# Optimization experiments

Measured on AMD Instinct MI355X. Metric: run time of the kernel, lower is better.

The kernel has to match this reference:

```python
import jax, jax.numpy as jnp
import numpy as np
import math

B, N, D, H, HC = 2, 2048, 1024, 16, 8
HIDDEN = 4 * D
MAX_PERIOD = 10000.0


def _timestep_embedding(t, dim):
    half = dim // 2
    freqs = jnp.exp(-math.log(MAX_PERIOD) * jnp.arange(half, dtype=jnp.float32) / half)
    args = t[:, None] * freqs[None, :]
    return jnp.concatenate([jnp.cos(args), jnp.sin(args)], axis=-1)


def _layer_norm(x, scale, bias, eps=1e-6):
    mu = jnp.mean(x, axis=-1, keepdims=True)
    var = jnp.mean(jnp.square(x - mu), axis=-1, keepdims=True)
    return (x - mu) * jax.lax.rsqrt(var + eps) * scale + bias


def _modulate(x, shift, scale):
    return x * (1.0 + scale[:, None, :]) + shift[:, None, :]


def setup_inputs():
    key = jax.random.key(0)
    ks = jax.random.split(key, 16)

    def dense(k, fin, fout):
        return jax.random.normal(k, (fin, fout), dtype=jnp.float32) / np.sqrt(fin)

    return {
        'x': jax.random.normal(ks[0], (B, N, D), dtype=jnp.float32),
        't': jax.random.uniform(ks[1], (B,), dtype=jnp.float32) * 1000.0,
        'norm1_scale': jnp.ones((D,), jnp.float32),
        'norm1_bias': jnp.zeros((D,), jnp.float32),
        'norm2_scale': jnp.ones((D,), jnp.float32),
        'norm2_bias': jnp.zeros((D,), jnp.float32),
        'tc_w1': dense(ks[2], HIDDEN, HIDDEN),
        'tc_b1': jnp.zeros((HIDDEN,), jnp.float32),
        'tc_w2': dense(ks[3], HIDDEN, HIDDEN),
        'tc_b2': jnp.zeros((HIDDEN,), jnp.float32),
        'tc_wa': 0.02 * dense(ks[4], HIDDEN, 4 * D),
        'tc_ba': jnp.zeros((4 * D,), jnp.float32),
        'tc_wc': 0.02 * dense(ks[5], HIDDEN, 4 * D),
        'tc_bc': jnp.zeros((4 * D,), jnp.float32),
        'attn_qk_w': dense(ks[6], D, D),
        'attn_v_w': dense(ks[7], D, D),
        'attn_out_w': dense(ks[8], D, D),
        'doob_w': 0.02 * dense(ks[9], D, 1),
        'doob_b': jnp.zeros((1,), jnp.float32),
        'ch_qk_w': dense(ks[10], D, D),
        'ch_v_w': dense(ks[11], D, D),
        'ch_out_w': dense(ks[12], D, D),
        'tau': jnp.ones((HC, 1, 1), jnp.float32),
        'gamma1': 1e-4 * jnp.ones((D,), jnp.float32),
        'gamma2': 1e-4 * jnp.ones((D,), jnp.float32),
    }


def reference(x, t, norm1_scale, norm1_bias, norm2_scale, norm2_bias,
              tc_w1, tc_b1, tc_w2, tc_b2, tc_wa, tc_ba, tc_wc, tc_bc,
              attn_qk_w, attn_v_w, attn_out_w, doob_w, doob_b,
              ch_qk_w, ch_v_w, ch_out_w, tau, gamma1, gamma2):
    # ---- AdaLN time conditioning ----
    emb = _timestep_embedding(t, HIDDEN)                 # (B, HIDDEN)
    h = jax.nn.silu(emb @ tc_w1 + tc_b1)
    h = jax.nn.silu(h @ tc_w2 + tc_b2)
    a_shift, a_scale, a_gate, a_lg = jnp.split(h @ tc_wa + tc_ba, 4, axis=-1)
    c_shift, c_scale, c_gate, c_lg = jnp.split(h @ tc_wc + tc_bc, 4, axis=-1)

    # ---- token-diffusion attention (MHDM, tied Q=K, Doob tilt) ----
    x1 = _modulate(_layer_norm(x, norm1_scale, norm1_bias), a_shift, a_scale)
    qk = (x1 @ attn_qk_w) * jnp.exp(a_lg)[:, None, :]    # (B,N,D)
    v = x1 @ attn_v_w
    dh = D // H
    qh = qk.reshape(B, N, H, dh).transpose(0, 2, 1, 3)   # (B,H,N,dh)
    vh = v.reshape(B, N, H, dh).transpose(0, 2, 1, 3)
    dot = jnp.einsum('bhmd,bhnd->bhmn', qh, qh)
    q2 = jnp.sum(qh * qh, axis=-1)
    logits = 2.0 * dot - q2[:, :, :, None] - q2[:, :, None, :]
    phi = (x1 @ doob_w + doob_b)[..., 0]                 # (B,N) destination tilt
    logits = logits + phi[:, None, None, :]
    attn = jax.nn.softmax(logits, axis=-1)
    w = jnp.einsum('bhmn,bhnd->bhmd', attn, vh)
    attn_out = w.transpose(0, 2, 1, 3).reshape(B, N, D) @ attn_out_w
    x = x + attn_out * a_gate[:, None, :] * gamma1

    # ---- channel-diffusion attention ----
    x2 = _modulate(_layer_norm(x, norm2_scale, norm2_bias), c_shift, c_scale)
    qkc = (x2 @ ch_qk_w) * jnp.exp(c_lg)[:, None, :]
    vc = x2 @ ch_v_w
    dhc = D // HC
    qkc = qkc.transpose(0, 2, 1).reshape(B, HC, dhc, N)  # (B,HC,dhc,N)
    vc = vc.transpose(0, 2, 1).reshape(B, HC, dhc, N)
    dotc = jnp.einsum('bhcn,bhdn->bhcd', qkc, qkc)
    q2c = jnp.sum(qkc * qkc, axis=-1)                    # (B,HC,dhc)
    logitsc = (2.0 * dotc - q2c[:, :, :, None] - q2c[:, :, None, :]) / math.sqrt(N)
    logitsc = logitsc * tau[None, ...]
    attnc = jax.nn.softmax(logitsc, axis=-1)
    wc = jnp.einsum('bhcd,bhdn->bhcn', attnc, vc)
    ch_out = wc.reshape(B, D, N).transpose(0, 2, 1) @ ch_out_w
    x = x + ch_out * c_gate[:, None, :] * gamma2
    return x
```

## Files before the change

### kernel.cpp

```cpp
#include <hip/hip_runtime.h>
#include <hip/hip_bf16.h>
#include <math.h>

typedef __bf16 bf16;
typedef bf16 bf16x8 __attribute__((ext_vector_type(8)));
typedef float f32x4 __attribute__((ext_vector_type(4)));

#define B_   2
#define N_   2048
#define D_   1024
#define H_   16
#define HC_  8
#define M_   (B_*N_)

__device__ __forceinline__ void gl16(const bf16* g, bf16* lds_base) {
#if __has_builtin(__builtin_amdgcn_global_load_lds)
  __builtin_amdgcn_global_load_lds((const __attribute__((address_space(1))) void*)g,
                                   (__attribute__((address_space(3))) void*)lds_base,
                                   16, 0, 0);
#else
  int lane = threadIdx.x & 63;
  *(uint4*)(lds_base + lane * 8) = *(const uint4*)g;
#endif
}

__global__ __launch_bounds__(256) void emb_kernel(const float* __restrict__ tin,
                                                  float* __restrict__ emb) {
  int idx = blockIdx.x * 256 + threadIdx.x;
  int b = idx >> 12, p = idx & 4095;
  float tv = tin[b];
  int half = p & 2047;
  float freq = expf(-logf(10000.f) * (float)half * (1.f / 2048.f));
  float arg = tv * freq;
  emb[idx] = (p < 2048) ? cosf(arg) : sinf(arg);
}

__global__ __launch_bounds__(256) void gemv_kernel(const float* __restrict__ x,
                                                   const float* __restrict__ W,
                                                   float* __restrict__ part) {
  __shared__ float xs[2][128];
  int t = threadIdx.x;
  int j0 = blockIdx.x * 512;
  int k0 = blockIdx.y * 128;
  if (t < 128) xs[0][t] = x[k0 + t];
  else         xs[1][t - 128] = x[4096 + k0 + (t - 128)];
  __syncthreads();
  float a00 = 0.f, a01 = 0.f, a10 = 0.f, a11 = 0.f;
  int j = j0 + t * 2;
  #pragma unroll 8
  for (int k = 0; k < 128; k++) {
    float2 wv = *(const float2*)(W + (size_t)(k0 + k) * 4096 + j);
    float x0 = xs[0][k], x1 = xs[1][k];
    a00 += x0 * wv.x; a01 += x0 * wv.y;
    a10 += x1 * wv.x; a11 += x1 * wv.y;
  }
  *(float2*)(part + (size_t)(blockIdx.y * 2 + 0) * 4096 + j) = make_float2(a00, a01);
  *(float2*)(part + (size_t)(blockIdx.y * 2 + 1) * 4096 + j) = make_float2(a10, a11);
}

__global__ __launch_bounds__(256) void gemv_reduce_kernel(const float* __restrict__ part,
                                                          const float* __restrict__ bias,
                                                          float* __restrict__ y, int act) {
  int idx = blockIdx.x * 256 + threadIdx.x;
  int b = idx >> 12, j = idx & 4095;
  float s = bias[j];
  #pragma unroll
  for (int kc = 0; kc < 32; kc++) s += part[(size_t)(kc * 2 + b) * 4096 + j];
  if (act) s = s / (1.f + expf(-s));
  y[idx] = s;
}

__global__ __launch_bounds__(256) void postA_kernel(const float* __restrict__ avec,
                                                    const float* __restrict__ cvec,
                                                    const float* __restrict__ g1,
                                                    const float* __restrict__ g2,
                                                    float* __restrict__ sca, float* __restrict__ scc,
                                                    float* __restrict__ agv, float* __restrict__ cgv) {
  int idx = blockIdx.x * 256 + threadIdx.x;
  int b = idx >> 10, d = idx & 1023;
  sca[idx] = expf(avec[b * 4096 + 3072 + d]);
  scc[idx] = expf(cvec[b * 4096 + 3072 + d]);
  agv[idx] = avec[b * 4096 + 2048 + d] * g1[d];
  cgv[idx] = cvec[b * 4096 + 2048 + d] * g2[d];
}

__global__ __launch_bounds__(256) void wtconv6_kernel(const float* w0, const float* w1,
                                                      const float* w2, const float* w3,
                                                      const float* w4, const float* w5,
                                                      bf16* o0, bf16* o1, bf16* o2,
                                                      bf16* o3, bf16* o4, bf16* o5) {
  const float* W; bf16* Wt;
  switch (blockIdx.z) {
    case 0: W = w0; Wt = o0; break;
    case 1: W = w1; Wt = o1; break;
    case 2: W = w2; Wt = o2; break;
    case 3: W = w3; Wt = o3; break;
    case 4: W = w4; Wt = o4; break;
    default: W = w5; Wt = o5; break;
  }
  __shared__ float tile[32][33];
  int t = threadIdx.x;
  int i = t >> 5, j = t & 31;
  int n0 = blockIdx.x * 32, k0 = blockIdx.y * 32;
  #pragma unroll
  for (int u = 0; u < 4; u++) {
    int k = i + u * 8;
    tile[k][j] = W[(size_t)(k0 + k) * 1024 + n0 + j];
  }
  __syncthreads();
  #pragma unroll
  for (int u = 0; u < 4; u++) {
    int n = i + u * 8;
    Wt[(size_t)(n0 + n) * 1024 + k0 + j] = (bf16)tile[j][n];
  }
}

__global__ __launch_bounds__(256) void ln_mod_kernel(const float* __restrict__ xin,
                                                     const float* __restrict__ nsc,
                                                     const float* __restrict__ nbi,
                                                     const float* __restrict__ mod,
                                                     const float* __restrict__ doobw,
                                                     float* __restrict__ phi,
                                                     bf16* __restrict__ outp) {
  int row = blockIdx.x;
  int b = row >> 11;
  int t = threadIdx.x;
  const float* xr = xin + (size_t)row * 1024;
  float v[4], s = 0.f, ss = 0.f;
  #pragma unroll
  for (int u = 0; u < 4; u++) { v[u] = xr[t + u * 256]; s += v[u]; ss += v[u] * v[u]; }
  #pragma unroll
  for (int off = 1; off < 64; off <<= 1) { s += __shfl_xor(s, off, 64); ss += __shfl_xor(ss, off, 64); }
  __shared__ float sb[4], ssb[4], pb[4];
  if ((t & 63) == 0) { sb[t >> 6] = s; ssb[t >> 6] = ss; }
  __syncthreads();
  s = sb[0] + sb[1] + sb[2] + sb[3];
  ss = ssb[0] + ssb[1] + ssb[2] + ssb[3];
  float mu = s * (1.f / 1024.f);
  float var = ss * (1.f / 1024.f) - mu * mu;
  float rs = rsqrtf(var + 1e-6f);
  const float* shv = mod + b * 4096;
  const float* scv = mod + b * 4096 + 1024;
  float ph = 0.f;
  #pragma unroll
  for (int u = 0; u < 4; u++) {
    int d = t + u * 256;
    float y = (v[u] - mu) * rs * nsc[d] + nbi[d];
    float ym = y * (1.f + scv[d]) + shv[d];
    outp[(size_t)row * 1024 + d] = (bf16)ym;
    if (doobw) ph += ym * doobw[d];
  }
  if (doobw) {
    #pragma unroll
    for (int off = 1; off < 64; off <<= 1) ph += __shfl_xor(ph, off, 64);
    if ((t & 63) == 0) pb[t >> 6] = ph;
    __syncthreads();
    if (t == 0) phi[row] = pb[0] + pb[1] + pb[2] + pb[3];
  }
}

__global__ __launch_bounds__(256) void phimax_kernel(const float* __restrict__ phi,
                                                     float* __restrict__ pm) {
  int b = blockIdx.x;
  int t = threadIdx.x;
  float m = -1e30f;
  #pragma unroll
  for (int u = 0; u < 8; u++) m = fmaxf(m, phi[b * 2048 + t + u * 256]);
  #pragma unroll
  for (int off = 1; off < 64; off <<= 1) m = fmaxf(m, __shfl_xor(m, off, 64));
  __shared__ float mb[4];
  if ((t & 63) == 0) mb[t >> 6] = m;
  __syncthreads();
  if (t == 0) pm[b] = fmaxf(fmaxf(mb[0], mb[1]), fmaxf(mb[2], mb[3]));
}

template <int MODE, int TM>
__global__ __launch_bounds__(256) void gemm_kernel(const bf16* __restrict__ A,
                                                   const bf16* __restrict__ Wt,
                                                   const float* __restrict__ scale,
                                                   const float* __restrict__ resid,
                                                   void* __restrict__ out0,
                                                   void* __restrict__ out1) {
  constexpr int K = 1024;
  constexpr int WM = TM / 2;
  constexpr int IT = WM / 16;
  __shared__ bf16 As[TM * 64];
  __shared__ bf16 Bs[128 * 64];
  const int m0 = blockIdx.x * TM;
  const int n0 = blockIdx.y * 128;
  const int t = threadIdx.x, lane = t & 63, wid = t >> 6;
  const int wy = wid >> 1, wx = wid & 1;
  const int ml = lane & 15, quad = lane >> 4, rq = quad * 4, kq = quad * 8;
  const int srow = lane >> 3;
  const int schunk = (lane & 7) ^ srow;
  const bf16* gA = A  + (size_t)(m0 + wid * (TM / 4) + srow) * K + schunk * 8;
  const bf16* gB = Wt + (size_t)(n0 + wid * 32 + srow) * K + schunk * 8;
  bf16* lA = As + (wid * (TM / 4)) * 64;
  bf16* lB = Bs + (wid * 32) * 64;
  const int mlm = ml & 7;

  f32x4 acc[IT][4] = {};
  for (int k0 = 0; k0 < K; k0 += 64) {
    __syncthreads();
    #pragma unroll
    for (int q = 0; q < TM / 32; q++)
      gl16(gA + (size_t)q * 8 * K + k0, lA + q * 8 * 64);
    #pragma unroll
    for (int q = 0; q < 4; q++)
      gl16(gB + (size_t)q * 8 * K + k0, lB + q * 8 * 64);
    __syncthreads();
    #pragma unroll
    for (int ks = 0; ks < 2; ks++) {
      const int slot = ((ks * 4 + quad) ^ mlm) * 8;
      bf16x8 af[IT], bfv[4];
      #pragma unroll
      for (int i = 0; i < IT; i++)
        af[i] = *(const bf16x8*)(As + (wy * WM + i * 16 + ml) * 64 + slot);
      #pragma unroll
      for (int j = 0; j < 4; j++)
        bfv[j] = *(const bf16x8*)(Bs + (wx * 64 + j * 16 + ml) * 64 + slot);
      #pragma unroll
      for (int i = 0; i < IT; i++)
        #pragma unroll
        for (int j = 0; j < 4; j++)
          acc[i][j] = __builtin_amdgcn_mfma_f32_16x16x32_bf16(af[i], bfv[j], acc[i][j], 0, 0, 0);
    }
  }
  #pragma unroll
  for (int i = 0; i < IT; i++) {
    #pragma unroll
    for (int j = 0; j < 4; j++) {
      int col = n0 + wx * 64 + j * 16 + ml;
      #pragma unroll
      for (int r = 0; r < 4; r++) {
        int row = m0 + wy * WM + i * 16 + rq + r;
        int b = row >> 11, n = row & 2047;
        float val = acc[i][j][r];
        if constexpr (MODE == 10) {
          if (col < 1024) {
            ((bf16*)out0)[(size_t)row * 1024 + col] = (bf16)(val * scale[b * 1024 + col]);
          } else {
            int c2 = col - 1024;
            ((bf16*)out1)[((size_t)((b * 16 + (c2 >> 6)) * 64 + (c2 & 63))) * 2048 + n] = (bf16)val;
          }
        } else if constexpr (MODE == 11) {
          if (col < 1024) {
            float sv = val * scale[b * 1024 + col];
            ((bf16*)out0)[((size_t)((b * 8 + (col >> 7)) * 128 + (col & 127))) * 2048 + n] = (bf16)sv;
          } else {
            ((bf16*)out1)[(size_t)row * 1024 + (col - 1024)] = (bf16)val;
          }
        } else {
          float g = scale[b * 1024 + col];
          ((float*)out0)[(size_t)row * 1024 + col] =
              resid[(size_t)row * 1024 + col] + val * g;
        }
      }
    }
  }
}

__global__ __launch_bounds__(256) void q2e_kernel(const bf16* __restrict__ qk,
                                                  const float* __restrict__ phi,
                                                  const float* __restrict__ pm,
                                                  float* __restrict__ q2buf,
                                                  float* __restrict__ ebuf) {
  int row = blockIdx.x;
  int b = row >> 11, n = row & 2047;
  int t = threadIdx.x;
  const bf16* qr = qk + (size_t)row * 1024;
  __shared__ float q2s[16][17];
  {
    int h = t >> 4, i0 = (t & 15) * 4;
    float q = 0.f;
    #pragma unroll
    for (int u = 0; u < 4; u++) { float qv = (float)qr[h * 64 + i0 + u]; q += qv * qv; }
    q2s[h][t & 15] = q;
  }
  __syncthreads();
  if (t < 16) {
    float q2 = 0.f;
    #pragma unroll
    for (int u = 0; u < 16; u++) q2 += q2s[t][u];
    q2buf[(size_t)(b * 16 + t) * 2048 + n] = q2;
    ebuf [(size_t)(b * 16 + t) * 2048 + n] = phi[row] - q2 - pm[b];
  }
}

__global__ __launch_bounds__(256) void flash_kernel(const bf16* __restrict__ qk,
                                                    const bf16* __restrict__ vt,
                                                    const float* __restrict__ q2buf,
                                                    const float* __restrict__ ebuf,
                                                    bf16* __restrict__ wout) {
  int mt = blockIdx.x, bh = blockIdx.y;
  int b = bh >> 4, h = bh & 15;
  int m0 = mt * 64;
  int t = threadIdx.x, lane = t & 63, w = t >> 6;
  int ml = lane & 15, kq = (lane >> 4) * 8, rq = (lane >> 4) * 4;

  __shared__ bf16 Qs[64 * 72];
  __shared__ bf16 Ks[64 * 72];
  __shared__ bf16 Vs[64 * 72];
  __shared__ bf16 Ps[64 * 72];

  #pragma unroll
  for (int u = 0; u < 2; u++) {
    int idx = u * 256 + t;
    int r = idx >> 3, seg = (idx & 7) * 8;
    *(uint4*)(Qs + r * 72 + seg) =
        *(const uint4*)(qk + (size_t)(b * 2048 + m0 + r) * 1024 + h * 64 + seg);
  }
  float q2l[4], rsum[4];
  const float* q2p = q2buf + (size_t)bh * 2048 + m0;
  #pragma unroll
  for (int r = 0; r < 4; r++) {
    q2l[r] = q2p[w * 16 + rq + r] * 1.44269504f;
    rsum[r] = 0.f;
  }
  f32x4 oacc[4] = {};
  const float* ep = ebuf + (size_t)bh * 2048;

  for (int nc = 0; nc < 32; nc++) {
    int n0c = nc * 64;
    __syncthreads();
    #pragma unroll
    for (int u = 0; u < 2; u++) {
      int idx = u * 256 + t;
      int r = idx >> 3, seg = (idx & 7) * 8;
      *(uint4*)(Ks + r * 72 + seg) =
          *(const uint4*)(qk + (size_t)(b * 2048 + n0c + r) * 1024 + h * 64 + seg);
      *(uint4*)(Vs + r * 72 + seg) =
          *(const uint4*)(vt + (size_t)(bh * 64 + r) * 2048 + n0c + seg);
    }
    __syncthreads();

    f32x4 sacc[4] = {};
    #pragma unroll
    for (int ks = 0; ks < 2; ks++) {
      bf16x8 qa = *(const bf16x8*)(Qs + (w * 16 + ml) * 72 + ks * 32 + kq);
      #pragma unroll
      for (int j = 0; j < 4; j++) {
        bf16x8 kb = *(const bf16x8*)(Ks + (j * 16 + ml) * 72 + ks * 32 + kq);
        sacc[j] = __builtin_amdgcn_mfma_f32_16x16x32_bf16(qa, kb, sacc[j], 0, 0, 0);
      }
    }

    float ejs[4];
    #pragma unroll
    for (int j = 0; j < 4; j++) ejs[j] = ep[n0c + j * 16 + ml] * 1.44269504f;
    #pragma unroll
    for (int r = 0; r < 4; r++) {
      int prow = (w * 16 + rq + r) * 72;
      float ps = 0.f;
      #pragma unroll
      for (int j = 0; j < 4; j++) {
        float p = exp2f(fmaf(2.88539008f, sacc[j][r], ejs[j] - q2l[r]));
        Ps[prow + j * 16 + ml] = (bf16)p;
        ps += p;
      }
      rsum[r] += ps;
    }
    #pragma unroll
    for (int ks = 0; ks < 2; ks++) {
      bf16x8 pa = *(const bf16x8*)(Ps + (w * 16 + ml) * 72 + ks * 32 + kq);
      #pragma unroll
      for (int jd = 0; jd < 4; jd++) {
        bf16x8 vb = *(const bf16x8*)(Vs + (jd * 16 + ml) * 72 + ks * 32 + kq);
        oacc[jd] = __builtin_amdgcn_mfma_f32_16x16x32_bf16(pa, vb, oacc[jd], 0, 0, 0);
      }
    }
  }
  #pragma unroll
  for (int r = 0; r < 4; r++) {
    rsum[r] += __shfl_xor(rsum[r], 1, 64);
    rsum[r] += __shfl_xor(rsum[r], 2, 64);
    rsum[r] += __shfl_xor(rsum[r], 4, 64);
    rsum[r] += __shfl_xor(rsum[r], 8, 64);
    rsum[r] = 1.f / rsum[r];
  }
  #pragma unroll
  for (int jd = 0; jd < 4; jd++)
    #pragma unroll
    for (int r = 0; r < 4; r++) {
      int row = w * 16 + rq + r;
      wout[(size_t)(b * 2048 + m0 + row) * 1024 + h * 64 + jd * 16 + ml] =
          (bf16)(oacc[jd][r] * rsum[r]);
    }
}

__global__ __launch_bounds__(256) void gram_kernel(const bf16* __restrict__ qkct,
                                                   float* __restrict__ dotp) {
  int bh = blockIdx.x, ksl = blockIdx.y;
  const bf16* Q = qkct + (size_t)bh * 128 * 2048 + ksl * 256;
  __shared__ bf16 Ts[128 * 40];
  int t = threadIdx.x, lane = t & 63, w = t >> 6;
  int ml = lane & 15, kq = (lane >> 4) * 8, rq = (lane >> 4) * 4;
  f32x4 acc[2][8] = {};
  for (int k0 = 0; k0 < 256; k0 += 32) {
    __syncthreads();
    #pragma unroll
    for (int u = 0; u < 2; u++) {
      int idx = u * 256 + t;
      int r = idx >> 2, seg = (idx & 3) * 8;
      *(uint4*)(Ts + r * 40 + seg) = *(const uint4*)(Q + (size_t)r * 2048 + k0 + seg);
    }
    __syncthreads();
    bf16x8 afr[2], bfr[8];
    #pragma unroll
    for (int i = 0; i < 2; i++) afr[i] = *(const bf16x8*)(Ts + (w * 32 + i * 16 + ml) * 40 + kq);
    #pragma unroll
    for (int j = 0; j < 8; j++) bfr[j] = *(const bf16x8*)(Ts + (j * 16 + ml) * 40 + kq);
    #pragma unroll
    for (int i = 0; i < 2; i++)
      #pragma unroll
      for (int j = 0; j < 8; j++)
        acc[i][j] = __builtin_amdgcn_mfma_f32_16x16x32_bf16(afr[i], bfr[j], acc[i][j], 0, 0, 0);
  }
  float* outp = dotp + ((size_t)ksl * 16 + bh) * 16384;
  #pragma unroll
  for (int i = 0; i < 2; i++)
    #pragma unroll
    for (int j = 0; j < 8; j++)
      #pragma unroll
      for (int r = 0; r < 4; r++) {
        int c = w * 32 + i * 16 + rq + r, d = j * 16 + ml;
        outp[c * 128 + d] = acc[i][j][r];
      }
}

__global__ __launch_bounds__(128) void chsm_kernel(const float* __restrict__ dotp,
                                                   const float* __restrict__ tau,
                                                   bf16* __restrict__ attnc) {
  int blk = blockIdx.x;
  int bh = blk >> 7, c = blk & 127, hc = bh & 7;
  int d = threadIdx.x;
  float dot = 0.f, dd = 0.f;
  #pragma unroll
  for (int kc = 0; kc < 8; kc++) {
    const float* pp = dotp + ((size_t)kc * 16 + bh) * 16384;
    dot += pp[c * 128 + d];
    dd  += pp[d * 128 + d];
  }
  __shared__ float diag[128];
  __shared__ float red[2], red2[2];
  diag[d] = dd;
  __syncthreads();
  float qc = diag[c];
  float sc = tau[hc] * rsqrtf(2048.f);
  float lg = sc * (2.f * dot - qc - dd);
  float mx = lg;
  #pragma unroll
  for (int off = 1; off < 64; off <<= 1) mx = fmaxf(mx, __shfl_xor(mx, off, 64));
  if ((d & 63) == 0) red[d >> 6] = mx;
  __syncthreads();
  mx = fmaxf(red[0], red[1]);
  float e = exp2f((lg - mx) * 1.44269504f);
  float sm = e;
  #pragma unroll
  for (int off = 1; off < 64; off <<= 1) sm += __shfl_xor(sm, off, 64);
  if ((d & 63) == 0) red2[d >> 6] = sm;
  __syncthreads();
  sm = red2[0] + red2[1];
  attnc[(size_t)bh * 16384 + c * 128 + d] = (bf16)(e / sm);
}

__global__ __launch_bounds__(256) void chav_kernel(const bf16* __restrict__ attnc,
                                                   const bf16* __restrict__ vc,
                                                   bf16* __restrict__ wcn) {
  int nb = blockIdx.x, bh = blockIdx.y;
  int b = bh >> 3, hc = bh & 7;
  int n0 = nb * 64;
  __shared__ bf16 As[128 * 136];
  __shared__ bf16 Bs[64 * 136];
  int t = threadIdx.x, lane = t & 63, w = t >> 6;
  int ml = lane & 15, kq = (lane >> 4) * 8, rq = (lane >> 4) * 4;
  #pragma unroll
  for (int u = 0; u < 8; u++) {
    int idx = u * 256 + t;
    int r = idx >> 4, seg = (idx & 15) * 8;
    *(uint4*)(As + r * 136 + seg) = *(const uint4*)(attnc + (size_t)bh * 16384 + r * 128 + seg);
  }
  #pragma unroll
  for (int u = 0; u < 4; u++) {
    int idx = u * 256 + t;
    int r = idx >> 4, seg = (idx & 15) * 8;
    *(uint4*)(Bs + r * 136 + seg) =
        *(const uint4*)(vc + (size_t)(b * 2048 + n0 + r) * 1024 + hc * 128 + seg);
  }
  __syncthreads();
  f32x4 acc[2][4] = {};
  #pragma unroll
  for (int ks = 0; ks < 4; ks++) {
    bf16x8 afr[2], bfr[4];
    #pragma unroll
    for (int i = 0; i < 2; i++)
      afr[i] = *(const bf16x8*)(As + (w * 32 + i * 16 + ml) * 136 + ks * 32 + kq);
    #pragma unroll
    for (int j = 0; j < 4; j++)
      bfr[j] = *(const bf16x8*)(Bs + (j * 16 + ml) * 136 + ks * 32 + kq);
    #pragma unroll
    for (int i = 0; i < 2; i++)
      #pragma unroll
      for (int j = 0; j < 4; j++)
        acc[i][j] = __builtin_amdgcn_mfma_f32_16x16x32_bf16(afr[i], bfr[j], acc[i][j], 0, 0, 0);
  }
  #pragma unroll
  for (int i = 0; i < 2; i++)
    #pragma unroll
    for (int j = 0; j < 4; j++)
      #pragma unroll
      for (int r = 0; r < 4; r++) {
        int c = w * 32 + i * 16 + rq + r;
        int n = n0 + j * 16 + ml;
        wcn[(size_t)(b * 2048 + n) * 1024 + hc * 128 + c] = (bf16)acc[i][j][r];
      }
}

extern "C" void kernel_launch(void* const* d_in, const int* in_sizes, int n_in,
                              void* d_out, int out_size, void* d_ws, size_t ws_size,
                              hipStream_t stream) {
  const float* x      = (const float*)d_in[0];
  const float* t      = (const float*)d_in[1];
  const float* n1s    = (const float*)d_in[2];
  const float* n1b    = (const float*)d_in[3];
  const float* n2s    = (const float*)d_in[4];
  const float* n2b    = (const float*)d_in[5];
  const float* tc_w1  = (const float*)d_in[6];
  const float* tc_b1  = (const float*)d_in[7];
  const float* tc_w2  = (const float*)d_in[8];
  const float* tc_b2  = (const float*)d_in[9];
  const float* tc_wa  = (const float*)d_in[10];
  const float* tc_ba  = (const float*)d_in[11];
  const float* tc_wc  = (const float*)d_in[12];
  const float* tc_bc  = (const float*)d_in[13];
  const float* aqk_w  = (const float*)d_in[14];
  const float* av_w   = (const float*)d_in[15];
  const float* aout_w = (const float*)d_in[16];
  const float* doobw  = (const float*)d_in[17];
  const float* cqk_w  = (const float*)d_in[19];
  const float* cv_w   = (const float*)d_in[20];
  const float* cout_w = (const float*)d_in[21];
  const float* tau    = (const float*)d_in[22];
  const float* g1     = (const float*)d_in[23];
  const float* g2     = (const float*)d_in[24];
  float* out = (float*)d_out;

  char* p = (char*)d_ws;
  auto alloc = [&](size_t bytes) -> void* {
    void* r = (void*)p;
    p += (bytes + 255) & ~(size_t)255;
    return r;
  };
  float* emb   = (float*)alloc(2 * 4096 * 4);
  float* partA = (float*)alloc(32 * 2 * 4096 * 4);
  float* partB = (float*)alloc(32 * 2 * 4096 * 4);
  float* h1    = (float*)alloc(2 * 4096 * 4);
  float* h2    = (float*)alloc(2 * 4096 * 4);
  float* avec  = (float*)alloc(2 * 4096 * 4);
  float* cvec  = (float*)alloc(2 * 4096 * 4);
  float* sca   = (float*)alloc(2 * 1024 * 4);
  float* scc   = (float*)alloc(2 * 1024 * 4);
  float* agv   = (float*)alloc(2 * 1024 * 4);
  float* cgv   = (float*)alloc(2 * 1024 * 4);
  float* phi   = (float*)alloc(4096 * 4);
  float* pmax  = (float*)alloc(2 * 4);
  float* q2buf = (float*)alloc(2 * 16 * 2048 * 4);
  float* ebuf  = (float*)alloc(2 * 16 * 2048 * 4);
  float* dotp  = (float*)alloc((size_t)8 * 16 * 16384 * 4);
  bf16* attnc  = (bf16*)alloc(16 * 128 * 128 * 2);
  bf16* wt     = (bf16*)alloc((size_t)6 * 1024 * 1024 * 2);
  bf16* xbf    = (bf16*)alloc((size_t)M_ * 1024 * 2);
  bf16* qkbf   = (bf16*)alloc((size_t)M_ * 1024 * 2);
  bf16* vbuf   = (bf16*)alloc((size_t)M_ * 1024 * 2);
  bf16* wbuf   = (bf16*)alloc((size_t)M_ * 1024 * 2);
  (void)ws_size; (void)in_sizes; (void)n_in; (void)out_size;

  bf16* wt_tok  = wt;
  bf16* wt_out  = wt + (size_t)2 * 1048576;
  bf16* wt_ch   = wt + (size_t)3 * 1048576;
  bf16* wt_cout = wt + (size_t)5 * 1048576;

  dim3 blk(256);
  wtconv6_kernel<<<dim3(32, 32, 6), blk, 0, stream>>>(
      aqk_w, av_w, aout_w, cqk_w, cv_w, cout_w,
      wt_tok, wt_tok + (size_t)1048576, wt_out,
      wt_ch,  wt_ch  + (size_t)1048576, wt_cout);

  emb_kernel<<<32, blk, 0, stream>>>(t, emb);
  gemv_kernel<<<dim3(8, 32), blk, 0, stream>>>(emb, tc_w1, partA);
  gemv_reduce_kernel<<<32, blk, 0, stream>>>(partA, tc_b1, h1, 1);
  gemv_kernel<<<dim3(8, 32), blk, 0, stream>>>(h1, tc_w2, partA);
  gemv_reduce_kernel<<<32, blk, 0, stream>>>(partA, tc_b2, h2, 1);
  gemv_kernel<<<dim3(8, 32), blk, 0, stream>>>(h2, tc_wa, partA);
  gemv_kernel<<<dim3(8, 32), blk, 0, stream>>>(h2, tc_wc, partB);
  gemv_reduce_kernel<<<32, blk, 0, stream>>>(partA, tc_ba, avec, 0);
  gemv_reduce_kernel<<<32, blk, 0, stream>>>(partB, tc_bc, cvec, 0);
  postA_kernel<<<8, blk, 0, stream>>>(avec, cvec, g1, g2, sca, scc, agv, cgv);

  ln_mod_kernel<<<4096, blk, 0, stream>>>(x, n1s, n1b, avec, doobw, phi, xbf);
  phimax_kernel<<<2, blk, 0, stream>>>(phi, pmax);
  gemm_kernel<10, 128><<<dim3(32, 16), blk, 0, stream>>>(xbf, wt_tok, sca, nullptr, qkbf, vbuf);
  q2e_kernel<<<4096, blk, 0, stream>>>(qkbf, phi, pmax, q2buf, ebuf);
  flash_kernel<<<dim3(32, 32), blk, 0, stream>>>(qkbf, vbuf, q2buf, ebuf, wbuf);
  gemm_kernel<4, 64><<<dim3(64, 8), blk, 0, stream>>>(wbuf, wt_out, agv, x, out, nullptr);

  ln_mod_kernel<<<4096, blk, 0, stream>>>(out, n2s, n2b, cvec, nullptr, nullptr, xbf);
  gemm_kernel<11, 128><<<dim3(32, 16), blk, 0, stream>>>(xbf, wt_ch, scc, nullptr, qkbf, vbuf);
  gram_kernel<<<dim3(16, 8), blk, 0, stream>>>(qkbf, dotp);
  chsm_kernel<<<2048, dim3(128), 0, stream>>>(dotp, tau, attnc);
  chav_kernel<<<dim3(32, 16), blk, 0, stream>>>(attnc, vbuf, wbuf);
  gemm_kernel<4, 64><<<dim3(64, 8), blk, 0, stream>>>(wbuf, wt_cout, cgv, out, out, nullptr);
}
```

Baseline: 592.0 us.

## Double-buffer flash attention with async LDS loads, swizzled layout, larger query tiles

The flash attention kernel now processes 128 query rows per 512-thread block. It keeps Q in registers, double-buffers K/V tiles in XOR-swizzled LDS via direct global-to-LDS loads, and computes transposed scores so each lane handles one query row. The log2e scaling moves into q2e_kernel, and P is packed to bf16 with v_cvt_pk_bf16_f32. Separately, the time-conditioning GEMV splits K across twice as many blocks and reuses the dotp buffer for partials. This should hide global load latency and cut LDS bank conflicts and one barrier per iteration, at the cost of more complex indexing and higher register pressure under launch_bounds(512,4).

```diff
diff --git a/kernel.cpp b/kernel.cpp
--- a/kernel.cpp
+++ b/kernel.cpp
@@ -4,6 +4,7 @@
 
 typedef __bf16 bf16;
 typedef bf16 bf16x8 __attribute__((ext_vector_type(8)));
+typedef bf16 bf16x2 __attribute__((ext_vector_type(2)));
 typedef float f32x4 __attribute__((ext_vector_type(4)));
 
 #define B_   2
@@ -24,6 +25,14 @@
 #endif
 }
 
+__device__ __forceinline__ bf16x2 cvt_pk_bf16(float lo, float hi) {
+  unsigned int r;
+  asm("v_cvt_pk_bf16_f32 %0, %1, %2" : "=v"(r) : "v"(lo), "v"(hi));
+  union { unsigned int u; bf16x2 v; } c;
+  c.u = r;
+  return c.v;
+}
+
 __global__ __launch_bounds__(256) void emb_kernel(const float* __restrict__ tin,
                                                   float* __restrict__ emb) {
   int idx = blockIdx.x * 256 + threadIdx.x;
@@ -38,17 +47,17 @@
 __global__ __launch_bounds__(256) void gemv_kernel(const float* __restrict__ x,
                                                    const float* __restrict__ W,
                                                    float* __restrict__ part) {
-  __shared__ float xs[2][128];
+  __shared__ float xs[2][64];
   int t = threadIdx.x;
   int j0 = blockIdx.x * 512;
-  int k0 = blockIdx.y * 128;
-  if (t < 128) xs[0][t] = x[k0 + t];
-  else         xs[1][t - 128] = x[4096 + k0 + (t - 128)];
+  int k0 = blockIdx.y * 64;
+  if (t < 64) xs[0][t] = x[k0 + t];
+  else if (t < 128) xs[1][t - 64] = x[4096 + k0 + (t - 64)];
   __syncthreads();
   float a00 = 0.f, a01 = 0.f, a10 = 0.f, a11 = 0.f;
   int j = j0 + t * 2;
   #pragma unroll 8
-  for (int k = 0; k < 128; k++) {
+  for (int k = 0; k < 64; k++) {
     float2 wv = *(const float2*)(W + (size_t)(k0 + k) * 4096 + j);
     float x0 = xs[0][k], x1 = xs[1][k];
     a00 += x0 * wv.x; a01 += x0 * wv.y;
@@ -65,7 +74,7 @@
   int b = idx >> 12, j = idx & 4095;
   float s = bias[j];
   #pragma unroll
-  for (int kc = 0; kc < 32; kc++) s += part[(size_t)(kc * 2 + b) * 4096 + j];
+  for (int kc = 0; kc < 64; kc++) s += part[(size_t)(kc * 2 + b) * 4096 + j];
   if (act) s = s / (1.f + expf(-s));
   y[idx] = s;
 }
@@ -282,110 +291,112 @@
     float q2 = 0.f;
     #pragma unroll
     for (int u = 0; u < 16; u++) q2 += q2s[t][u];
-    q2buf[(size_t)(b * 16 + t) * 2048 + n] = q2;
-    ebuf [(size_t)(b * 16 + t) * 2048 + n] = phi[row] - q2 - pm[b];
-  }
-}
-
-__global__ __launch_bounds__(256) void flash_kernel(const bf16* __restrict__ qk,
-                                                    const bf16* __restrict__ vt,
-                                                    const float* __restrict__ q2buf,
-                                                    const float* __restrict__ ebuf,
-                                                    bf16* __restrict__ wout) {
+    q2buf[(size_t)(b * 16 + t) * 2048 + n] = q2 * 1.44269504f;
+    ebuf [(size_t)(b * 16 + t) * 2048 + n] = (phi[row] - q2 - pm[b]) * 1.44269504f;
+  }
+}
+
+__global__ __launch_bounds__(512, 4) void flash_kernel(const bf16* __restrict__ qk,
+                                                       const bf16* __restrict__ vt,
+                                                       const float* __restrict__ q2buf,
+                                                       const float* __restrict__ ebuf,
+                                                       bf16* __restrict__ wout) {
   int mt = blockIdx.x, bh = blockIdx.y;
   int b = bh >> 4, h = bh & 15;
-  int m0 = mt * 64;
+  int m0 = mt * 128;
   int t = threadIdx.x, lane = t & 63, w = t >> 6;
-  int ml = lane & 15, kq = (lane >> 4) * 8, rq = (lane >> 4) * 4;
-
-  __shared__ bf16 Qs[64 * 72];
-  __shared__ bf16 Ks[64 * 72];
-  __shared__ bf16 Vs[64 * 72];
-  __shared__ bf16 Ps[64 * 72];
-
-  #pragma unroll
-  for (int u = 0; u < 2; u++) {
-    int idx = u * 256 + t;
-    int r = idx >> 3, seg = (idx & 7) * 8;
-    *(uint4*)(Qs + r * 72 + seg) =
-        *(const uint4*)(qk + (size_t)(b * 2048 + m0 + r) * 1024 + h * 64 + seg);
-  }
-  float q2l[4], rsum[4];
-  const float* q2p = q2buf + (size_t)bh * 2048 + m0;
-  #pragma unroll
-  for (int r = 0; r < 4; r++) {
-    q2l[r] = q2p[w * 16 + rq + r] * 1.44269504f;
-    rsum[r] = 0.f;
-  }
+  int ml = lane & 15, quad = lane >> 4;
+  int mlm = ml & 7, q1 = quad & 1, qh = quad >> 1;
+
+  __shared__ __align__(16) bf16 Ks[2][64 * 64];
+  __shared__ __align__(16) bf16 Vs[2][64 * 64];
+  __shared__ __align__(16) bf16 Ps[8 * 16 * 64];
+
+  int sr = lane >> 3, swz = (lane & 7) ^ sr;
+  const bf16* gK = qk + (size_t)(b * 2048 + 8 * w + sr) * 1024 + h * 64 + swz * 8;
+  const bf16* gV = vt + (size_t)(bh * 64 + 8 * w + sr) * 2048 + swz * 8;
+
+  const bf16* qrow = qk + (size_t)(b * 2048 + m0 + w * 16 + ml) * 1024 + h * 64;
+  bf16x8 qf0 = *(const bf16x8*)(qrow + quad * 8);
+  bf16x8 qf1 = *(const bf16x8*)(qrow + 32 + quad * 8);
+
+  float q2l = q2buf[(size_t)bh * 2048 + m0 + w * 16 + ml];
+  const float* ep = ebuf + (size_t)bh * 2048;
+
+  bf16* Pb = Ps + (w * 16 + ml) * 64;
   f32x4 oacc[4] = {};
-  const float* ep = ebuf + (size_t)bh * 2048;
-
+  float rs = 0.f;
+
+  gl16(gK, &Ks[0][w * 512]);
+  gl16(gV, &Vs[0][w * 512]);
+
+  #pragma unroll 2
   for (int nc = 0; nc < 32; nc++) {
-    int n0c = nc * 64;
+    int cur = nc & 1;
     __syncthreads();
-    #pragma unroll
-    for (int u = 0; u < 2; u++) {
-      int idx = u * 256 + t;
-      int r = idx >> 3, seg = (idx & 7) * 8;
-      *(uint4*)(Ks + r * 72 + seg) =
-          *(const uint4*)(qk + (size_t)(b * 2048 + n0c + r) * 1024 + h * 64 + seg);
-      *(uint4*)(Vs + r * 72 + seg) =
-          *(const uint4*)(vt + (size_t)(bh * 64 + r) * 2048 + n0c + seg);
+    if (nc + 1 < 32) {
+      gl16(gK + (size_t)(nc + 1) * 64 * 1024, &Ks[cur ^ 1][w * 512]);
+      gl16(gV + (nc + 1) * 64,                &Vs[cur ^ 1][w * 512]);
     }
-    __syncthreads();
+    const bf16* Kc = Ks[cur];
+    const bf16* Vc = Vs[cur];
 
     f32x4 sacc[4] = {};
+    __builtin_amdgcn_s_setprio(1);
     #pragma unroll
     for (int ks = 0; ks < 2; ks++) {
-      bf16x8 qa = *(const bf16x8*)(Qs + (w * 16 + ml) * 72 + ks * 32 + kq);
+      bf16x8 qb = ks ? qf1 : qf0;
       #pragma unroll
       for (int j = 0; j < 4; j++) {
-        bf16x8 kb = *(const bf16x8*)(Ks + (j * 16 + ml) * 72 + ks * 32 + kq);
-        sacc[j] = __builtin_amdgcn_mfma_f32_16x16x32_bf16(qa, kb, sacc[j], 0, 0, 0);
+        bf16x8 ka = *(const bf16x8*)(Kc + (j * 16 + ml) * 64 + ((4 * ks + quad) ^ mlm) * 8);
+        sacc[j] = __builtin_amdgcn_mfma_f32_16x16x32_bf16(ka, qb, sacc[j], 0, 0, 0);
       }
     }
-
-    float ejs[4];
-    #pragma unroll
-    for (int j = 0; j < 4; j++) ejs[j] = ep[n0c + j * 16 + ml] * 1.44269504f;
-    #pragma unroll
-    for (int r = 0; r < 4; r++) {
-      int prow = (w * 16 + rq + r) * 72;
-      float ps = 0.f;
-      #pragma unroll
-      for (int j = 0; j < 4; j++) {
-        float p = exp2f(fmaf(2.88539008f, sacc[j][r], ejs[j] - q2l[r]));
-        Ps[prow + j * 16 + ml] = (bf16)p;
-        ps += p;
-      }
-      rsum[r] += ps;
+    __builtin_amdgcn_s_setprio(0);
+
+    const float* epc = ep + nc * 64;
+    #pragma unroll
+    for (int j = 0; j < 4; j++) {
+      float4 ev = *(const float4*)(epc + j * 16 + quad * 4);
+      float p0 = exp2f(fmaf(2.88539008f, sacc[j][0], ev.x - q2l));
+      float p1 = exp2f(fmaf(2.88539008f, sacc[j][1], ev.y - q2l));
+      float p2 = exp2f(fmaf(2.88539008f, sacc[j][2], ev.z - q2l));
+      float p3 = exp2f(fmaf(2.88539008f, sacc[j][3], ev.w - q2l));
+      rs += (p0 + p1) + (p2 + p3);
+      int sl = (((2 * j + qh) ^ mlm) * 4 + 2 * q1) * 2;
+      *(bf16x2*)(Pb + sl)     = cvt_pk_bf16(p0, p1);
+      *(bf16x2*)(Pb + sl + 2) = cvt_pk_bf16(p2, p3);
     }
+    __builtin_amdgcn_sched_barrier(0);
+
+    __builtin_amdgcn_s_setprio(1);
     #pragma unroll
     for (int ks = 0; ks < 2; ks++) {
-      bf16x8 pa = *(const bf16x8*)(Ps + (w * 16 + ml) * 72 + ks * 32 + kq);
+      bf16x8 pa = *(const bf16x8*)(Pb + ((4 * ks + quad) ^ mlm) * 8);
       #pragma unroll
       for (int jd = 0; jd < 4; jd++) {
-        bf16x8 vb = *(const bf16x8*)(Vs + (jd * 16 + ml) * 72 + ks * 32 + kq);
+        bf16x8 vb = *(const bf16x8*)(Vc + (jd * 16 + ml) * 64 + ((4 * ks + quad) ^ mlm) * 8);
         oacc[jd] = __builtin_amdgcn_mfma_f32_16x16x32_bf16(pa, vb, oacc[jd], 0, 0, 0);
       }
     }
-  }
-  #pragma unroll
-  for (int r = 0; r < 4; r++) {
-    rsum[r] += __shfl_xor(rsum[r], 1, 64);
-    rsum[r] += __shfl_xor(rsum[r], 2, 64);
-    rsum[r] += __shfl_xor(rsum[r], 4, 64);
-    rsum[r] += __shfl_xor(rsum[r], 8, 64);
-    rsum[r] = 1.f / rsum[r];
-  }
+    __builtin_amdgcn_s_setprio(0);
+  }
+
+  rs += __shfl_xor(rs, 16, 64);
+  rs += __shfl_xor(rs, 32, 64);
+  float rinv = 1.f / rs;
+
+  int rq = quad * 4;
+  float rv[4];
+  #pragma unroll
+  for (int r = 0; r < 4; r++) rv[r] = __shfl(rinv, rq + r, 64);
+
+  bf16* wrow = wout + (size_t)(b * 2048 + m0 + w * 16) * 1024 + h * 64;
   #pragma unroll
   for (int jd = 0; jd < 4; jd++)
     #pragma unroll
-    for (int r = 0; r < 4; r++) {
-      int row = w * 16 + rq + r;
-      wout[(size_t)(b * 2048 + m0 + row) * 1024 + h * 64 + jd * 16 + ml] =
-          (bf16)(oacc[jd][r] * rsum[r]);
-    }
+    for (int r = 0; r < 4; r++)
+      wrow[(size_t)(rq + r) * 1024 + jd * 16 + ml] = (bf16)(oacc[jd][r] * rv[r]);
 }
 
 __global__ __launch_bounds__(256) void gram_kernel(const bf16* __restrict__ qkct,
@@ -552,8 +563,6 @@
     return r;
   };
   float* emb   = (float*)alloc(2 * 4096 * 4);
-  float* partA = (float*)alloc(32 * 2 * 4096 * 4);
-  float* partB = (float*)alloc(32 * 2 * 4096 * 4);
   float* h1    = (float*)alloc(2 * 4096 * 4);
   float* h2    = (float*)alloc(2 * 4096 * 4);
   float* avec  = (float*)alloc(2 * 4096 * 4);
@@ -575,6 +584,9 @@
   bf16* wbuf   = (bf16*)alloc((size_t)M_ * 1024 * 2);
   (void)ws_size; (void)in_sizes; (void)n_in; (void)out_size;
 
+  float* partA = dotp;
+  float* partB = dotp + (size_t)64 * 2 * 4096;
+
   bf16* wt_tok  = wt;
   bf16* wt_out  = wt + (size_t)2 * 1048576;
   bf16* wt_ch   = wt + (size_t)3 * 1048576;
@@ -587,12 +599,12 @@
       wt_ch,  wt_ch  + (size_t)1048576, wt_cout);
 
   emb_kernel<<<32, blk, 0, stream>>>(t, emb);
-  gemv_kernel<<<dim3(8, 32), blk, 0, stream>>>(emb, tc_w1, partA);
+  gemv_kernel<<<dim3(8, 64), blk, 0, stream>>>(emb, tc_w1, partA);
   gemv_reduce_kernel<<<32, blk, 0, stream>>>(partA, tc_b1, h1, 1);
-  gemv_kernel<<<dim3(8, 32), blk, 0, stream>>>(h1, tc_w2, partA);
+  gemv_kernel<<<dim3(8, 64), blk, 0, stream>>>(h1, tc_w2, partA);
   gemv_reduce_kernel<<<32, blk, 0, stream>>>(partA, tc_b2, h2, 1);
-  gemv_kernel<<<dim3(8, 32), blk, 0, stream>>>(h2, tc_wa, partA);
-  gemv_kernel<<<dim3(8, 32), blk, 0, stream>>>(h2, tc_wc, partB);
+  gemv_kernel<<<dim3(8, 64), blk, 0, stream>>>(h2, tc_wa, partA);
+  gemv_kernel<<<dim3(8, 64), blk, 0, stream>>>(h2, tc_wc, partB);
   gemv_reduce_kernel<<<32, blk, 0, stream>>>(partA, tc_ba, avec, 0);
   gemv_reduce_kernel<<<32, blk, 0, stream>>>(partB, tc_bc, cvec, 0);
   postA_kernel<<<8, blk, 0, stream>>>(avec, cvec, g1, g2, sca, scc, agv, cgv);
@@ -601,7 +613,7 @@
   phimax_kernel<<<2, blk, 0, stream>>>(phi, pmax);
   gemm_kernel<10, 128><<<dim3(32, 16), blk, 0, stream>>>(xbf, wt_tok, sca, nullptr, qkbf, vbuf);
   q2e_kernel<<<4096, blk, 0, stream>>>(qkbf, phi, pmax, q2buf, ebuf);
-  flash_kernel<<<dim3(32, 32), blk, 0, stream>>>(qkbf, vbuf, q2buf, ebuf, wbuf);
+  flash_kernel<<<dim3(16, 32), dim3(512), 0, stream>>>(qkbf, vbuf, q2buf, ebuf, wbuf);
   gemm_kernel<4, 64><<<dim3(64, 8), blk, 0, stream>>>(wbuf, wt_out, agv, x, out, nullptr);
 
   ln_mod_kernel<<<4096, blk, 0, stream>>>(out, n2s, n2b, cvec, nullptr, nullptr, xbf);
```

New measurement: 643.1 us. +8.6%, slower.
